# Performance work log

Hardware: AMD Instinct MI355X
Metric: run time of the kernel (lower is better)

## Reference

```python
import jax, jax.numpy as jnp
import numpy as np

B, H, T, D = 2, 16, 2048, 64


def setup_inputs() -> dict:
    key = jax.random.key(0)
    kq, kk, kv, km = jax.random.split(key, 4)
    q = jax.random.normal(kq, (B, H, T, D), dtype=jnp.float32)
    k = jax.random.normal(kk, (B, H, T, D), dtype=jnp.float32)
    v = jax.random.normal(kv, (B, H, T, D), dtype=jnp.float32)
    # boolean mask, True = masked out (broadcast over batch and heads)
    mask = jax.random.randint(km, (1, 1, T, T), 0, 2).astype(jnp.bool_)
    return {"q": q, "k": k, "v": v, "mask": mask}


def reference(q, k, v, mask):
    scale = q.shape[-1] ** (-0.5)
    # [B,H,T,T] score matrix (materialized, as in the original)
    scores = jnp.einsum("bhqd,bhkd->bhqk", q, k) * scale
    scores = jnp.where(mask, jnp.float32(-10000.0), scores)
    attn = jax.nn.softmax(scores, axis=-1)
    attn = jnp.where(mask, jnp.float32(0.0), attn)
    return jnp.einsum("bhqk,bhkd->bhqd", attn, v)
```

## Files before the change

kernel.cpp:

```cpp
#include <hip/hip_runtime.h>
#include <hip/hip_bf16.h>

typedef __bf16 bf16x8 __attribute__((ext_vector_type(8)));
typedef __bf16 bf16x4 __attribute__((ext_vector_type(4)));
typedef float  f32x4  __attribute__((ext_vector_type(4)));
typedef short  s16x4  __attribute__((ext_vector_type(4)));

#define T_SEQ 2048
#define D_HEAD 64
#define BH_N 32
#define SCALE_LOG2 0.18033688011112042f

#define WS_KBF ((size_t)0)
#define WS_VTB ((size_t)8u<<20)
#define WS_MB  ((size_t)16u<<20)

static __device__ inline f32x4 mfma16(bf16x4 a, bf16x4 b, f32x4 c) {
#if __has_builtin(__builtin_amdgcn_mfma_f32_16x16x16_bf16)
    return __builtin_amdgcn_mfma_f32_16x16x16_bf16(a, b, c, 0, 0, 0);
#else
    s16x4 ai = __builtin_bit_cast(s16x4, a);
    s16x4 bi = __builtin_bit_cast(s16x4, b);
    return __builtin_amdgcn_mfma_f32_16x16x16bf16_1k(ai, bi, c, 0, 0, 0);
#endif
}

static __device__ inline float fast_exp2(float x) {
#if __has_builtin(__builtin_amdgcn_exp2f)
    return __builtin_amdgcn_exp2f(x);
#else
    return exp2f(x);
#endif
}


__global__ __launch_bounds__(256) void prep_kv(const float* __restrict__ k,
                                               const float* __restrict__ v,
                                               __bf16* __restrict__ kb,
                                               __bf16* __restrict__ vt) {
    __shared__ __bf16 t[64][72];
    const int bh = blockIdx.y, tt = blockIdx.x, tid = threadIdx.x;
    {
        const size_t base = ((size_t)bh * T_SEQ + tt * 64 + (tid >> 2)) * D_HEAD + (tid & 3) * 16;
        const float4 a0 = *(const float4*)(k + base);
        const float4 a1 = *(const float4*)(k + base + 4);
        const float4 a2 = *(const float4*)(k + base + 8);
        const float4 a3 = *(const float4*)(k + base + 12);
        bf16x8 w0, w1;
        w0[0]=(__bf16)a0.x; w0[1]=(__bf16)a0.y; w0[2]=(__bf16)a0.z; w0[3]=(__bf16)a0.w;
        w0[4]=(__bf16)a1.x; w0[5]=(__bf16)a1.y; w0[6]=(__bf16)a1.z; w0[7]=(__bf16)a1.w;
        w1[0]=(__bf16)a2.x; w1[1]=(__bf16)a2.y; w1[2]=(__bf16)a2.z; w1[3]=(__bf16)a2.w;
        w1[4]=(__bf16)a3.x; w1[5]=(__bf16)a3.y; w1[6]=(__bf16)a3.z; w1[7]=(__bf16)a3.w;
        *(bf16x8*)(kb + base)     = w0;
        *(bf16x8*)(kb + base + 8) = w1;
    }
    {
        const int tr = tid >> 4, c4 = (tid & 15) * 4;
        const float* src = v + ((size_t)bh * T_SEQ + tt * 64) * D_HEAD;
#pragma unroll
        for (int p = 0; p < 4; ++p) {
            const int row = p * 16 + tr;
            const float4 f = *(const float4*)(src + row * D_HEAD + c4);
            t[c4+0][row] = (__bf16)f.x; t[c4+1][row] = (__bf16)f.y;
            t[c4+2][row] = (__bf16)f.z; t[c4+3][row] = (__bf16)f.w;
        }
        __syncthreads();
        const int d = tid >> 2, seg = tid & 3;
        const bf16x8 a = *(bf16x8*)&t[d][seg * 16];
        const bf16x8 b = *(bf16x8*)&t[d][seg * 16 + 8];
        __bf16* dst = vt + ((size_t)bh * D_HEAD + d) * T_SEQ + tt * 64 + seg * 16;
        *(bf16x8*)dst = a; *(bf16x8*)(dst + 8) = b;
    }
}

__global__ void mpack(const int* __restrict__ m, unsigned long long* __restrict__ mb) {
    const int i = blockIdx.x * 256 + threadIdx.x;
    const unsigned long long b = __ballot(m[i] != 0);
    if ((threadIdx.x & 63) == 0) mb[i >> 6] = b;
}


__global__ __launch_bounds__(256, 4) void attn8(
    const float* __restrict__ q, const __bf16* __restrict__ kb,
    const __bf16* __restrict__ vt, const unsigned long long* __restrict__ mb,
    float* __restrict__ out)
{
    const int qt = blockIdx.x;
    const int bh = blockIdx.y;
    const int tid = threadIdx.x, wave = tid >> 6, lane = tid & 63;
    const int g = lane >> 4, ln = lane & 15;
    const int qp = wave & 1, kh = wave >> 1;

    __shared__ __align__(16) char smem[33280];
    char* KlB = smem;
    char* VlB = smem + 16384;
    float* Ep = (float*)smem;
    float* Os = (float*)(smem + 32768);

    const int qw = qt * 64 + qp * 32;

    bf16x8 qf[2][2];
#pragma unroll
    for (int qs = 0; qs < 2; ++qs) {
        const float* qpt = q + ((size_t)bh * T_SEQ + qw + qs * 16 + ln) * D_HEAD + g * 8;
#pragma unroll
        for (int kc = 0; kc < 2; ++kc) {
            const float4 f0 = *(const float4*)(qpt + kc * 32);
            const float4 f1 = *(const float4*)(qpt + kc * 32 + 4);
            qf[qs][kc][0]=(__bf16)(f0.x*SCALE_LOG2); qf[qs][kc][1]=(__bf16)(f0.y*SCALE_LOG2);
            qf[qs][kc][2]=(__bf16)(f0.z*SCALE_LOG2); qf[qs][kc][3]=(__bf16)(f0.w*SCALE_LOG2);
            qf[qs][kc][4]=(__bf16)(f1.x*SCALE_LOG2); qf[qs][kc][5]=(__bf16)(f1.y*SCALE_LOG2);
            qf[qs][kc][6]=(__bf16)(f1.z*SCALE_LOG2); qf[qs][kc][7]=(__bf16)(f1.w*SCALE_LOG2);
        }
    }

    f32x4 o[2][4];
#pragma unroll
    for (int qs = 0; qs < 2; ++qs)
#pragma unroll
        for (int mt = 0; mt < 4; ++mt) o[qs][mt] = (f32x4){0.f, 0.f, 0.f, 0.f};
    f32x4 osum[2] = { (f32x4){0.f,0.f,0.f,0.f}, (f32x4){0.f,0.f,0.f,0.f} };
    const bf16x4 ones = { (__bf16)1.0f, (__bf16)1.0f, (__bf16)1.0f, (__bf16)1.0f };

    const int kr = tid >> 2, qd = tid & 3;
    const int kwb = kr * 128, ke = kr & 7;
    const __bf16* kbase = kb + (size_t)bh * T_SEQ * D_HEAD;
    const __bf16* vbase = vt + (size_t)bh * D_HEAD * T_SEQ;
    const unsigned long long* mrow0 = mb + (size_t)(qw + ln) * 32;
    const unsigned long long* mrow1 = mb + (size_t)(qw + 16 + ln) * 32;

    bf16x8 kn[2], vn[2];

    {
        const __bf16* kp = kbase + (size_t)kr * D_HEAD + qd * 16;
        kn[0] = *(const bf16x8*)kp; kn[1] = *(const bf16x8*)(kp + 8);
        const __bf16* vp = vbase + (size_t)kr * T_SEQ + qd * 16;
        vn[0] = *(const bf16x8*)vp; vn[1] = *(const bf16x8*)(vp + 8);
    }
    unsigned long long mw0 = mrow0[0], mw1 = mrow1[0];
    {
        *(bf16x8*)(KlB + kwb + (((2*qd + 0) ^ ke) << 4)) = kn[0];
        *(bf16x8*)(KlB + kwb + (((2*qd + 1) ^ ke) << 4)) = kn[1];
#pragma unroll
        for (int c = 0; c < 2; ++c)
#pragma unroll
            for (int gg = 0; gg < 2; ++gg) {
                const int g2 = c * 2 + gg;
                const int gran = (g2 << 1) | (qd >> 1);
                const bf16x4 part = gg ? __builtin_shufflevector(vn[c], vn[c], 4,5,6,7)
                                       : __builtin_shufflevector(vn[c], vn[c], 0,1,2,3);
                *(bf16x4*)(VlB + kwb + ((gran ^ ke) << 4) + ((qd & 1) << 3)) = part;
            }
    }
    __syncthreads();

    for (int kt = 0; kt < T_SEQ / 64; ++kt) {
        const int b = kt & 1;
        unsigned long long mn0 = 0, mn1 = 0;
        if (kt < 31) {
            const __bf16* kp = kbase + (size_t)((kt + 1) * 64 + kr) * D_HEAD + qd * 16;
            kn[0] = *(const bf16x8*)kp; kn[1] = *(const bf16x8*)(kp + 8);
            const __bf16* vp = vbase + (size_t)kr * T_SEQ + (kt + 1) * 64 + qd * 16;
            vn[0] = *(const bf16x8*)vp; vn[1] = *(const bf16x8*)(vp + 8);
            mn0 = mrow0[kt + 1]; mn1 = mrow1[kt + 1];
        }

        const char* KB = KlB + b * 8192;
        const char* VB = VlB + b * 8192;

        const unsigned nbs0 = (~(unsigned)(mw0 >> (kh << 5))) >> (g * 4);
        const unsigned nbs1 = (~(unsigned)(mw1 >> (kh << 5))) >> (g * 4);

        bf16x4 pa[2][2];
#pragma unroll
        for (int ntl = 0; ntl < 2; ++ntl) {
            const int row = (2 * kh + ntl) * 16 + ln;
            const int rb = row * 128 + ((g ^ (ln & 7)) << 4);
            const bf16x8 a0 = *(const bf16x8*)(KB + rb);
            const bf16x8 a1 = *(const bf16x8*)(KB + (rb ^ 64));
#pragma unroll
            for (int qs = 0; qs < 2; ++qs) {
                f32x4 c = (f32x4){0.f, 0.f, 0.f, 0.f};
                c = __builtin_amdgcn_mfma_f32_16x16x32_bf16(a0, qf[qs][0], c, 0, 0, 0);
                c = __builtin_amdgcn_mfma_f32_16x16x32_bf16(a1, qf[qs][1], c, 0, 0, 0);
                const unsigned nbs = qs ? nbs1 : nbs0;
                float p[4];
#pragma unroll
                for (int r = 0; r < 4; ++r) {
                    const float e = fast_exp2(c[r]);
                    const int keep = (int)(nbs << (31 - (ntl * 16 + r))) >> 31;
                    p[r] = __builtin_bit_cast(float, __builtin_bit_cast(unsigned, e) & (unsigned)keep);
                }
                pa[qs][ntl] = (bf16x4){ (__bf16)p[0], (__bf16)p[1], (__bf16)p[2], (__bf16)p[3] };
                osum[qs] = mfma16(pa[qs][ntl], ones, osum[qs]);
            }
        }

#pragma unroll
        for (int mt = 0; mt < 4; ++mt) {
            const int vrow = mt * 16 + ln;
            const bf16x8 vv = *(const bf16x8*)(VB + vrow * 128 + ((((g << 1) | kh) ^ (ln & 7)) << 4));
            const bf16x4 vf0 = __builtin_shufflevector(vv, vv, 0, 1, 2, 3);
            const bf16x4 vf1 = __builtin_shufflevector(vv, vv, 4, 5, 6, 7);
#pragma unroll
            for (int qs = 0; qs < 2; ++qs) {
                o[qs][mt] = mfma16(pa[qs][0], vf0, o[qs][mt]);
                o[qs][mt] = mfma16(pa[qs][1], vf1, o[qs][mt]);
            }
        }

        if (kt < 31) {
            char* KB1 = KlB + (b ^ 1) * 8192;
            char* VB1 = VlB + (b ^ 1) * 8192;
            *(bf16x8*)(KB1 + kwb + (((2*qd + 0) ^ ke) << 4)) = kn[0];
            *(bf16x8*)(KB1 + kwb + (((2*qd + 1) ^ ke) << 4)) = kn[1];
#pragma unroll
            for (int c = 0; c < 2; ++c)
#pragma unroll
                for (int gg = 0; gg < 2; ++gg) {
                    const int g2 = c * 2 + gg;
                    const int gran = (g2 << 1) | (qd >> 1);
                    const bf16x4 part = gg ? __builtin_shufflevector(vn[c], vn[c], 4,5,6,7)
                                           : __builtin_shufflevector(vn[c], vn[c], 0,1,2,3);
                    *(bf16x4*)(VB1 + kwb + ((gran ^ ke) << 4) + ((qd & 1) << 3)) = part;
                }
        }
        __syncthreads();
        mw0 = mn0; mw1 = mn1;
    }

#pragma unroll
    for (int qs = 0; qs < 2; ++qs) {
#pragma unroll
        for (int mt = 0; mt < 4; ++mt)
#pragma unroll
            for (int r = 0; r < 4; ++r)
                Ep[(size_t)kh * 4096 + (qp * 32 + qs * 16 + g * 4 + r) * 64 + mt * 16 + ln] = o[qs][mt][r];
        if (ln == 0) {
#pragma unroll
            for (int r = 0; r < 4; ++r)
                Os[kh * 64 + qp * 32 + qs * 16 + g * 4 + r] = osum[qs][r];
        }
    }
    __syncthreads();
#pragma unroll
    for (int p = 0; p < 4; ++p) {
        const int idx = p * 256 + tid;
        const int row = idx >> 4, c4 = (idx & 15) * 4;
        const float l = Os[row] + Os[64 + row];
        const float inv = (l > 0.f) ? (1.f / l) : 0.f;
        const float4 a  = *(const float4*)(Ep + row * 64 + c4);
        const float4 b4 = *(const float4*)(Ep + 4096 + row * 64 + c4);
        const float4 st = { (a.x + b4.x) * inv, (a.y + b4.y) * inv,
                            (a.z + b4.z) * inv, (a.w + b4.w) * inv };
        *(float4*)(out + ((size_t)bh * T_SEQ + qt * 64 + row) * D_HEAD + c4) = st;
    }
}

extern "C" void kernel_launch(void* const* d_in, const int* in_sizes, int n_in,
                              void* d_out, int out_size, void* d_ws, size_t ws_size,
                              hipStream_t stream) {
    const float* q    = (const float*)d_in[0];
    const float* k    = (const float*)d_in[1];
    const float* v    = (const float*)d_in[2];
    const int*   mask = (const int*)d_in[3];
    float*       out  = (float*)d_out;

    __bf16* kbf = (__bf16*)((char*)d_ws + WS_KBF);
    __bf16* vtb = (__bf16*)((char*)d_ws + WS_VTB);
    unsigned long long* mbw = (unsigned long long*)((char*)d_ws + WS_MB);

    prep_kv<<<dim3(T_SEQ / 64, BH_N), 256, 0, stream>>>(k, v, kbf, vtb);
    mpack<<<(T_SEQ * T_SEQ) / 256, 256, 0, stream>>>(mask, mbw);
    attn8<<<dim3(T_SEQ / 64, BH_N), 256, 0, stream>>>(q, kbf, vtb, mbw, out);
}
```

Before: 167.7 us.

## Prebuild swizzled K/V tile images and stream them via direct global-to-LDS loads

The prep kernel now writes K and V for each 64-key tile into a contiguous 16KB block that already has the XOR-swizzled LDS layout. The attention kernel copies each block straight into shared memory with global_load_lds, double buffered, so it no longer stages data through registers and scatters it with swizzled stores. The P·V and row-sum MFMAs change from 16x16x16 to 16x16x32, halving the instruction count. The risk is that the direct-to-LDS loads are asynchronous, and the code depends on __syncthreads alone to make that data visible before it is read.

```diff
diff --git a/kernel.cpp b/kernel.cpp
--- a/kernel.cpp
+++ b/kernel.cpp
@@ -4,28 +4,22 @@
 typedef __bf16 bf16x8 __attribute__((ext_vector_type(8)));
 typedef __bf16 bf16x4 __attribute__((ext_vector_type(4)));
 typedef float  f32x4  __attribute__((ext_vector_type(4)));
-typedef short  s16x4  __attribute__((ext_vector_type(4)));
 
 #define T_SEQ 2048
 #define D_HEAD 64
 #define BH_N 32
+#define NT_TILES (T_SEQ / 64)
+#define IMG_BYTES 16384
 #define SCALE_LOG2 0.18033688011112042f
 
-#define WS_KBF ((size_t)0)
-#define WS_VTB ((size_t)8u<<20)
-#define WS_MB  ((size_t)16u<<20)
-
-static __device__ inline f32x4 mfma16(bf16x4 a, bf16x4 b, f32x4 c) {
-#if __has_builtin(__builtin_amdgcn_mfma_f32_16x16x16_bf16)
-    return __builtin_amdgcn_mfma_f32_16x16x16_bf16(a, b, c, 0, 0, 0);
-#else
-    s16x4 ai = __builtin_bit_cast(s16x4, a);
-    s16x4 bi = __builtin_bit_cast(s16x4, b);
-    return __builtin_amdgcn_mfma_f32_16x16x16bf16_1k(ai, bi, c, 0, 0, 0);
-#endif
-}
-
-static __device__ inline float fast_exp2(float x) {
+#define WS_IMG ((size_t)0)
+#define WS_MB  ((size_t)16u << 20)
+
+static __device__ __forceinline__ f32x4 mfma32(bf16x8 a, bf16x8 b, f32x4 c) {
+    return __builtin_amdgcn_mfma_f32_16x16x32_bf16(a, b, c, 0, 0, 0);
+}
+
+static __device__ __forceinline__ float fast_exp2(float x) {
 #if __has_builtin(__builtin_amdgcn_exp2f)
     return __builtin_amdgcn_exp2f(x);
 #else
@@ -33,15 +27,27 @@
 #endif
 }
 
+static __device__ __forceinline__ void gload16(const void* g, void* l, int lane) {
+#if __has_builtin(__builtin_amdgcn_global_load_lds)
+    (void)lane;
+    __builtin_amdgcn_global_load_lds(
+        (const __attribute__((address_space(1))) void*)g,
+        (__attribute__((address_space(3))) void*)l, 16, 0, 0);
+#else
+    *((f32x4*)l + lane) = *(const f32x4*)g;
+#endif
+}
+
 
 __global__ __launch_bounds__(256) void prep_kv(const float* __restrict__ k,
                                                const float* __restrict__ v,
-                                               __bf16* __restrict__ kb,
-                                               __bf16* __restrict__ vt) {
+                                               char* __restrict__ img) {
     __shared__ __bf16 t[64][72];
     const int bh = blockIdx.y, tt = blockIdx.x, tid = threadIdx.x;
+    char* ob = img + ((size_t)bh * NT_TILES + tt) * IMG_BYTES;
     {
-        const size_t base = ((size_t)bh * T_SEQ + tt * 64 + (tid >> 2)) * D_HEAD + (tid & 3) * 16;
+        const int kr = tid >> 2, qd = tid & 3, ke = kr & 7;
+        const size_t base = ((size_t)bh * T_SEQ + tt * 64 + kr) * D_HEAD + qd * 16;
         const float4 a0 = *(const float4*)(k + base);
         const float4 a1 = *(const float4*)(k + base + 4);
         const float4 a2 = *(const float4*)(k + base + 8);
@@ -51,8 +57,8 @@
         w0[4]=(__bf16)a1.x; w0[5]=(__bf16)a1.y; w0[6]=(__bf16)a1.z; w0[7]=(__bf16)a1.w;
         w1[0]=(__bf16)a2.x; w1[1]=(__bf16)a2.y; w1[2]=(__bf16)a2.z; w1[3]=(__bf16)a2.w;
         w1[4]=(__bf16)a3.x; w1[5]=(__bf16)a3.y; w1[6]=(__bf16)a3.z; w1[7]=(__bf16)a3.w;
-        *(bf16x8*)(kb + base)     = w0;
-        *(bf16x8*)(kb + base + 8) = w1;
+        *(bf16x8*)(ob + kr * 128 + (((2 * qd + 0) ^ ke) << 4)) = w0;
+        *(bf16x8*)(ob + kr * 128 + (((2 * qd + 1) ^ ke) << 4)) = w1;
     }
     {
         const int tr = tid >> 4, c4 = (tid & 15) * 4;
@@ -65,11 +71,17 @@
             t[c4+2][row] = (__bf16)f.z; t[c4+3][row] = (__bf16)f.w;
         }
         __syncthreads();
-        const int d = tid >> 2, seg = tid & 3;
-        const bf16x8 a = *(bf16x8*)&t[d][seg * 16];
-        const bf16x8 b = *(bf16x8*)&t[d][seg * 16 + 8];
-        __bf16* dst = vt + ((size_t)bh * D_HEAD + d) * T_SEQ + tt * 64 + seg * 16;
-        *(bf16x8*)dst = a; *(bf16x8*)(dst + 8) = b;
+        const int d = tid >> 2;
+        char* vb = ob + 8192 + d * 128;
+#pragma unroll
+        for (int mi = 0; mi < 2; ++mi) {
+            const int m  = (tid & 3) * 2 + mi;
+            const int u  = m ^ (d & 7);
+            const int k0 = (u & 1) * 32 + (u >> 1) * 4;
+            const bf16x4 lo = *(const bf16x4*)&t[d][k0];
+            const bf16x4 hi = *(const bf16x4*)&t[d][k0 + 16];
+            *(bf16x8*)(vb + m * 16) = __builtin_shufflevector(lo, hi, 0,1,2,3,4,5,6,7);
+        }
     }
 }
 
@@ -80,10 +92,9 @@
 }
 
 
-__global__ __launch_bounds__(256, 4) void attn8(
-    const float* __restrict__ q, const __bf16* __restrict__ kb,
-    const __bf16* __restrict__ vt, const unsigned long long* __restrict__ mb,
-    float* __restrict__ out)
+__global__ __launch_bounds__(256, 4) void attn9(
+    const float* __restrict__ q, const char* __restrict__ img,
+    const unsigned long long* __restrict__ mb, float* __restrict__ out)
 {
     const int qt = blockIdx.x;
     const int bh = blockIdx.y;
@@ -92,8 +103,6 @@
     const int qp = wave & 1, kh = wave >> 1;
 
     __shared__ __align__(16) char smem[33280];
-    char* KlB = smem;
-    char* VlB = smem + 16384;
     float* Ep = (float*)smem;
     float* Os = (float*)(smem + 32768);
 
@@ -120,58 +129,40 @@
 #pragma unroll
         for (int mt = 0; mt < 4; ++mt) o[qs][mt] = (f32x4){0.f, 0.f, 0.f, 0.f};
     f32x4 osum[2] = { (f32x4){0.f,0.f,0.f,0.f}, (f32x4){0.f,0.f,0.f,0.f} };
-    const bf16x4 ones = { (__bf16)1.0f, (__bf16)1.0f, (__bf16)1.0f, (__bf16)1.0f };
-
-    const int kr = tid >> 2, qd = tid & 3;
-    const int kwb = kr * 128, ke = kr & 7;
-    const __bf16* kbase = kb + (size_t)bh * T_SEQ * D_HEAD;
-    const __bf16* vbase = vt + (size_t)bh * D_HEAD * T_SEQ;
+    const bf16x8 ones8 = { (__bf16)1.0f, (__bf16)1.0f, (__bf16)1.0f, (__bf16)1.0f,
+                           (__bf16)1.0f, (__bf16)1.0f, (__bf16)1.0f, (__bf16)1.0f };
+
+    const char* ibase = img + (size_t)bh * (NT_TILES * (size_t)IMG_BYTES);
     const unsigned long long* mrow0 = mb + (size_t)(qw + ln) * 32;
     const unsigned long long* mrow1 = mb + (size_t)(qw + 16 + ln) * 32;
 
-    bf16x8 kn[2], vn[2];
-
     {
-        const __bf16* kp = kbase + (size_t)kr * D_HEAD + qd * 16;
-        kn[0] = *(const bf16x8*)kp; kn[1] = *(const bf16x8*)(kp + 8);
-        const __bf16* vp = vbase + (size_t)kr * T_SEQ + qd * 16;
-        vn[0] = *(const bf16x8*)vp; vn[1] = *(const bf16x8*)(vp + 8);
+        const char* src = ibase + wave * 4096 + lane * 16;
+        char* dst = smem + wave * 4096;
+#pragma unroll
+        for (int i = 0; i < 4; ++i) gload16(src + i * 1024, dst + i * 1024, lane);
     }
     unsigned long long mw0 = mrow0[0], mw1 = mrow1[0];
-    {
-        *(bf16x8*)(KlB + kwb + (((2*qd + 0) ^ ke) << 4)) = kn[0];
-        *(bf16x8*)(KlB + kwb + (((2*qd + 1) ^ ke) << 4)) = kn[1];
-#pragma unroll
-        for (int c = 0; c < 2; ++c)
-#pragma unroll
-            for (int gg = 0; gg < 2; ++gg) {
-                const int g2 = c * 2 + gg;
-                const int gran = (g2 << 1) | (qd >> 1);
-                const bf16x4 part = gg ? __builtin_shufflevector(vn[c], vn[c], 4,5,6,7)
-                                       : __builtin_shufflevector(vn[c], vn[c], 0,1,2,3);
-                *(bf16x4*)(VlB + kwb + ((gran ^ ke) << 4) + ((qd & 1) << 3)) = part;
-            }
-    }
     __syncthreads();
 
-    for (int kt = 0; kt < T_SEQ / 64; ++kt) {
+    for (int kt = 0; kt < NT_TILES; ++kt) {
         const int b = kt & 1;
         unsigned long long mn0 = 0, mn1 = 0;
-        if (kt < 31) {
-            const __bf16* kp = kbase + (size_t)((kt + 1) * 64 + kr) * D_HEAD + qd * 16;
-            kn[0] = *(const bf16x8*)kp; kn[1] = *(const bf16x8*)(kp + 8);
-            const __bf16* vp = vbase + (size_t)kr * T_SEQ + (kt + 1) * 64 + qd * 16;
-            vn[0] = *(const bf16x8*)vp; vn[1] = *(const bf16x8*)(vp + 8);
+        if (kt < NT_TILES - 1) {
+            const char* src = ibase + (size_t)(kt + 1) * IMG_BYTES + wave * 4096 + lane * 16;
+            char* dst = smem + (b ^ 1) * 16384 + wave * 4096;
+#pragma unroll
+            for (int i = 0; i < 4; ++i) gload16(src + i * 1024, dst + i * 1024, lane);
             mn0 = mrow0[kt + 1]; mn1 = mrow1[kt + 1];
         }
 
-        const char* KB = KlB + b * 8192;
-        const char* VB = VlB + b * 8192;
+        const char* KB = smem + b * 16384;
+        const char* VB = KB + 8192;
 
         const unsigned nbs0 = (~(unsigned)(mw0 >> (kh << 5))) >> (g * 4);
         const unsigned nbs1 = (~(unsigned)(mw1 >> (kh << 5))) >> (g * 4);
 
-        bf16x4 pa[2][2];
+        bf16x8 pa8[2];
 #pragma unroll
         for (int ntl = 0; ntl < 2; ++ntl) {
             const int row = (2 * kh + ntl) * 16 + ln;
@@ -181,50 +172,31 @@
 #pragma unroll
             for (int qs = 0; qs < 2; ++qs) {
                 f32x4 c = (f32x4){0.f, 0.f, 0.f, 0.f};
-                c = __builtin_amdgcn_mfma_f32_16x16x32_bf16(a0, qf[qs][0], c, 0, 0, 0);
-                c = __builtin_amdgcn_mfma_f32_16x16x32_bf16(a1, qf[qs][1], c, 0, 0, 0);
+                c = mfma32(a0, qf[qs][0], c);
+                c = mfma32(a1, qf[qs][1], c);
                 const unsigned nbs = qs ? nbs1 : nbs0;
-                float p[4];
 #pragma unroll
                 for (int r = 0; r < 4; ++r) {
                     const float e = fast_exp2(c[r]);
                     const int keep = (int)(nbs << (31 - (ntl * 16 + r))) >> 31;
-                    p[r] = __builtin_bit_cast(float, __builtin_bit_cast(unsigned, e) & (unsigned)keep);
+                    const float p = __builtin_bit_cast(float,
+                        __builtin_bit_cast(unsigned, e) & (unsigned)keep);
+                    pa8[qs][ntl * 4 + r] = (__bf16)p;
                 }
-                pa[qs][ntl] = (bf16x4){ (__bf16)p[0], (__bf16)p[1], (__bf16)p[2], (__bf16)p[3] };
-                osum[qs] = mfma16(pa[qs][ntl], ones, osum[qs]);
             }
         }
 
 #pragma unroll
+        for (int qs = 0; qs < 2; ++qs) osum[qs] = mfma32(pa8[qs], ones8, osum[qs]);
+#pragma unroll
         for (int mt = 0; mt < 4; ++mt) {
-            const int vrow = mt * 16 + ln;
-            const bf16x8 vv = *(const bf16x8*)(VB + vrow * 128 + ((((g << 1) | kh) ^ (ln & 7)) << 4));
-            const bf16x4 vf0 = __builtin_shufflevector(vv, vv, 0, 1, 2, 3);
-            const bf16x4 vf1 = __builtin_shufflevector(vv, vv, 4, 5, 6, 7);
-#pragma unroll
-            for (int qs = 0; qs < 2; ++qs) {
-                o[qs][mt] = mfma16(pa[qs][0], vf0, o[qs][mt]);
-                o[qs][mt] = mfma16(pa[qs][1], vf1, o[qs][mt]);
-            }
-        }
-
-        if (kt < 31) {
-            char* KB1 = KlB + (b ^ 1) * 8192;
-            char* VB1 = VlB + (b ^ 1) * 8192;
-            *(bf16x8*)(KB1 + kwb + (((2*qd + 0) ^ ke) << 4)) = kn[0];
-            *(bf16x8*)(KB1 + kwb + (((2*qd + 1) ^ ke) << 4)) = kn[1];
-#pragma unroll
-            for (int c = 0; c < 2; ++c)
-#pragma unroll
-                for (int gg = 0; gg < 2; ++gg) {
-                    const int g2 = c * 2 + gg;
-                    const int gran = (g2 << 1) | (qd >> 1);
-                    const bf16x4 part = gg ? __builtin_shufflevector(vn[c], vn[c], 4,5,6,7)
-                                           : __builtin_shufflevector(vn[c], vn[c], 0,1,2,3);
-                    *(bf16x4*)(VB1 + kwb + ((gran ^ ke) << 4) + ((qd & 1) << 3)) = part;
-                }
-        }
+            const bf16x8 vv = *(const bf16x8*)(VB + (mt * 16 + ln) * 128
+                                + ((((g << 1) | kh) ^ (ln & 7)) << 4));
+#pragma unroll
+            for (int qs = 0; qs < 2; ++qs)
+                o[qs][mt] = mfma32(pa8[qs], vv, o[qs][mt]);
+        }
+
         __syncthreads();
         mw0 = mn0; mw1 = mn1;
     }
@@ -266,11 +238,10 @@
     const int*   mask = (const int*)d_in[3];
     float*       out  = (float*)d_out;
 
-    __bf16* kbf = (__bf16*)((char*)d_ws + WS_KBF);
-    __bf16* vtb = (__bf16*)((char*)d_ws + WS_VTB);
+    char* img = (char*)d_ws + WS_IMG;
     unsigned long long* mbw = (unsigned long long*)((char*)d_ws + WS_MB);
 
-    prep_kv<<<dim3(T_SEQ / 64, BH_N), 256, 0, stream>>>(k, v, kbf, vtb);
+    prep_kv<<<dim3(NT_TILES, BH_N), 256, 0, stream>>>(k, v, img);
     mpack<<<(T_SEQ * T_SEQ) / 256, 256, 0, stream>>>(mask, mbw);
-    attn8<<<dim3(T_SEQ / 64, BH_N), 256, 0, stream>>>(q, kbf, vtb, mbw, out);
-}
+    attn9<<<dim3(NT_TILES, BH_N), 256, 0, stream>>>(q, img, mbw, out);
+}
```

New measurement: 161.3 us. 1.04x faster.
